# Performance work log

Measured on AMD Instinct MI355X. Metric: run time of the kernel, lower is better.

Reference implementation:

```python
import jax, jax.numpy as jnp
import numpy as np

LAM_U = 0.1
LAM_V = 0.1
LAM_P = 0.1
LAM_Q = 0.1

N_USERS, N_ITEMS, K = 8192, 8192, 256


def _trace(x):
    # PMF repos define trace(x) = sum of squared entries (Frobenius norm^2)
    return jnp.sum(x * x)


def setup_inputs() -> dict:
    key = jax.random.key(0)
    ks = jax.random.split(key, 8)
    R = jax.random.normal(ks[0], (N_USERS, N_ITEMS), jnp.float32)
    R = R * (jax.random.uniform(ks[1], (N_USERS, N_ITEMS)) < 0.05).astype(jnp.float32)
    Y = jax.random.normal(ks[2], (N_USERS, N_ITEMS), jnp.float32)
    Y = Y * (jax.random.uniform(ks[3], (N_USERS, N_ITEMS)) < 0.05).astype(jnp.float32)
    u_features = jax.random.normal(ks[4], (N_USERS, K), jnp.float32)
    v_features = jax.random.normal(ks[5], (N_ITEMS, K), jnp.float32)
    P = jax.random.normal(ks[6], (K, N_USERS), jnp.float32)
    Q = jax.random.normal(ks[7], (K, N_USERS), jnp.float32)
    alpha = jnp.float32(0.5)
    return {"R": R, "u_features": u_features, "v_features": v_features,
            "alpha": alpha, "Y": Y, "P": P, "Q": Q}


def reference(R, u_features, v_features, alpha, Y, P, Q):
    non_zero_mask = (R != 0).astype(jnp.float32)              # [U, I]
    # (P^T * u_features) @ v_features^T : low-rank predicted ratings [U, I]
    predicted = jnp.matmul(P.T * u_features, v_features.T)
    prediction_error = jnp.sum((R - predicted) ** 2 * non_zero_mask) / 2

    non_zero_mask_Y = (Y != 0).astype(jnp.float32)
    predicted_y = jnp.matmul(Q.T * u_features, v_features.T)
    prediction_error_y = alpha * jnp.sum((Y - predicted_y) ** 2 * non_zero_mask_Y) / 2  # computed but NOT returned (faithful to source)

    u_reg = LAM_U * _trace(u_features) / 2
    v_reg = LAM_V * _trace(v_features) / 2
    p_reg = LAM_P * _trace(P) / 2
    q_reg = LAM_Q * _trace(Q) / 2  # computed but not returned (faithful)
    return prediction_error + u_reg + v_reg + p_reg
```

## Files before the change

kernel.cpp:

```cpp
#include <hip/hip_runtime.h>
#include <hip/hip_bf16.h>

typedef __attribute__((ext_vector_type(8))) short short8;
typedef __attribute__((ext_vector_type(4))) float f32x4;

#define N_U 8192
#define N_I 8192
#define KD  256

#define ERR_SLOTS 8192
#define REGA_BASE 8192
#define REGV_BASE 8704
#define SLOTS_END 10752

#define GLD16(g, l) __builtin_amdgcn_global_load_lds( \
    (const __attribute__((address_space(1))) unsigned int*)(unsigned long long)(uintptr_t)(g), \
    (__attribute__((address_space(3))) unsigned int*)(unsigned int)(uintptr_t)(l), 16, 0, 0)

static __device__ __forceinline__ unsigned short f2bf(float x) {
  unsigned u = __builtin_bit_cast(unsigned, x);
  u += 0x7fffu + ((u >> 16) & 1u);
  return (unsigned short)(u >> 16);
}

static __device__ __forceinline__ void block_reduce_store(float v, float* slot) {
  #pragma unroll
  for (int off = 32; off > 0; off >>= 1) v += __shfl_down(v, off, 64);
  __shared__ float red[4];
  int lane = threadIdx.x & 63, wv = threadIdx.x >> 6;
  if (lane == 0) red[wv] = v;
  __syncthreads();
  if (threadIdx.x == 0) *slot = red[0] + red[1] + red[2] + red[3];
}

__global__ __launch_bounds__(256) void pack_a_kernel(
    const float* __restrict__ U, const float* __restrict__ P,
    unsigned short* __restrict__ Abf, float* __restrict__ ws)
{
  __shared__ float Pt[64][65];
  const int u0 = blockIdx.x * 64;
  const int k0 = blockIdx.y * 64;
  const int t = threadIdx.x;
  float ss = 0.f;
  {
    const int ul4 = (t & 15) * 4, klb = t >> 4;
    #pragma unroll
    for (int pass = 0; pass < 4; ++pass) {
      int kl = klb + pass * 16;
      float4 pv = *(const float4*)&P[(size_t)(k0 + kl) * N_U + u0 + ul4];
      Pt[kl][ul4 + 0] = pv.x; Pt[kl][ul4 + 1] = pv.y;
      Pt[kl][ul4 + 2] = pv.z; Pt[kl][ul4 + 3] = pv.w;
      ss += pv.x * pv.x + pv.y * pv.y + pv.z * pv.z + pv.w * pv.w;
    }
  }
  __syncthreads();
  {
    const int k4 = (t & 15) * 4, ulb = t >> 4;
    #pragma unroll
    for (int pass = 0; pass < 4; ++pass) {
      int ul = ulb + pass * 16;
      float4 uv = *(const float4*)&U[(size_t)(u0 + ul) * KD + k0 + k4];
      ss += uv.x * uv.x + uv.y * uv.y + uv.z * uv.z + uv.w * uv.w;
      ushort4 w;
      w.x = f2bf(uv.x * Pt[k4 + 0][ul]);
      w.y = f2bf(uv.y * Pt[k4 + 1][ul]);
      w.z = f2bf(uv.z * Pt[k4 + 2][ul]);
      w.w = f2bf(uv.w * Pt[k4 + 3][ul]);
      *(ushort4*)&Abf[(size_t)(u0 + ul) * KD + k0 + k4] = w;
    }
  }
  block_reduce_store(ss, ws + REGA_BASE + blockIdx.y * 128 + blockIdx.x);
}

__global__ __launch_bounds__(256) void pack_v_kernel(
    const float* __restrict__ V, unsigned short* __restrict__ Vbf,
    float* __restrict__ ws)
{
  size_t i = ((size_t)blockIdx.x * 256 + threadIdx.x) * 4;
  float4 v = *(const float4*)&V[i];
  float ss = v.x * v.x + v.y * v.y + v.z * v.z + v.w * v.w;
  ushort4 w;
  w.x = f2bf(v.x); w.y = f2bf(v.y); w.z = f2bf(v.z); w.w = f2bf(v.w);
  *(ushort4*)&Vbf[i] = w;
  block_reduce_store(ss, ws + REGV_BASE + blockIdx.x);
}

__global__ __launch_bounds__(256) void gemm_loss_kernel(
    const float* __restrict__ R, const unsigned short* __restrict__ Abf,
    const unsigned short* __restrict__ Vbf, float* __restrict__ ws)
{
  __shared__ unsigned short As[2][128 * 32];
  __shared__ unsigned short Bs[2][64 * 32];
  const int tid = threadIdx.x;
  const int wv = tid >> 6, lane = tid & 63;
  const int brow = blockIdx.x, bcol = blockIdx.y;
  const int wr = wv >> 1, wc = wv & 1;

  f32x4 acc[4][2] = {};
  float4 rreg[8];

  const unsigned short* Ag = Abf + (size_t)brow * 128 * KD;
  const unsigned short* Bg = Vbf + (size_t)bcol * 64 * KD;
  const int fa0 = tid, fa1 = tid + 256, fb = tid;
  const int r0 = lane & 15, kc = (lane >> 4) * 8;

  const int row0 = brow * 128 + wr * 64 + (lane & 15);
  const size_t col0 = (size_t)bcol * 64 + wc * 32 + (lane >> 4) * 4;
  const float* Rtile = R + (size_t)row0 * N_I + col0;

#define STAGE(buf, kt) do { \
    GLD16(Ag + ((fa0 >> 2) * KD + (kt) + (fa0 & 3) * 8), &As[buf][fa0 * 8]); \
    GLD16(Ag + ((fa1 >> 2) * KD + (kt) + (fa1 & 3) * 8), &As[buf][fa1 * 8]); \
    GLD16(Bg + ((fb  >> 2) * KD + (kt) + (fb  & 3) * 8), &Bs[buf][fb * 8]);  \
  } while (0)

  STAGE(0, 0);
  asm volatile("s_waitcnt vmcnt(0)" ::: "memory");
  __builtin_amdgcn_s_barrier();

  #pragma unroll
  for (int t = 0; t < 8; ++t) {
    const int cur = t & 1;
    if (t < 7) STAGE(cur ^ 1, (t + 1) * 32);
    rreg[t] = *(const float4*)(Rtile + (size_t)((t >> 1) * 16) * N_I + (t & 1) * 16);

    short8 a[4], b[2];
    #pragma unroll
    for (int m = 0; m < 4; ++m)
      a[m] = *(const short8*)&As[cur][(wr * 64 + m * 16 + r0) * 32 + kc];
    #pragma unroll
    for (int n = 0; n < 2; ++n)
      b[n] = *(const short8*)&Bs[cur][(wc * 32 + n * 16 + r0) * 32 + kc];
    #pragma unroll
    for (int m = 0; m < 4; ++m)
      #pragma unroll
      for (int n = 0; n < 2; ++n)
        acc[m][n] = __builtin_amdgcn_mfma_f32_16x16x32_bf16(b[n], a[m], acc[m][n], 0, 0, 0);

    asm volatile("s_waitcnt lgkmcnt(0) vmcnt(1)" ::: "memory");
    __builtin_amdgcn_s_barrier();
  }
#undef STAGE

  asm volatile("s_waitcnt vmcnt(0)" ::: "memory");
  float lsum = 0.f;
  #pragma unroll
  for (int t = 0; t < 8; ++t) {
    const int m = t >> 1, n = t & 1;
    float4 rv = rreg[t];
    if (rv.x != 0.f) { float d = rv.x - acc[m][n][0]; lsum += d * d; }
    if (rv.y != 0.f) { float d = rv.y - acc[m][n][1]; lsum += d * d; }
    if (rv.z != 0.f) { float d = rv.z - acc[m][n][2]; lsum += d * d; }
    if (rv.w != 0.f) { float d = rv.w - acc[m][n][3]; lsum += d * d; }
  }

  #pragma unroll
  for (int off = 32; off > 0; off >>= 1) lsum += __shfl_down(lsum, off, 64);
  float* red = (float*)As;
  __syncthreads();
  if (lane == 0) red[wv] = lsum;
  __syncthreads();
  if (tid == 0) ws[blockIdx.y * 64 + blockIdx.x] = red[0] + red[1] + red[2] + red[3];
}

__global__ __launch_bounds__(256) void finalize_kernel(
    const float* __restrict__ ws, float* __restrict__ out)
{
  __shared__ float sh[256];
  const int tid = threadIdx.x;
  float e = 0.f, r = 0.f;
  for (int i = tid; i < ERR_SLOTS; i += 256) e += ws[i];
  for (int i = REGA_BASE + tid; i < SLOTS_END; i += 256) r += ws[i];
  sh[tid] = 0.5f * e + 0.05f * r;
  __syncthreads();
  #pragma unroll
  for (int s = 128; s > 0; s >>= 1) {
    if (tid < s) sh[tid] += sh[tid + s];
    __syncthreads();
  }
  if (tid == 0) out[0] = sh[0];
}

extern "C" void kernel_launch(void* const* d_in, const int* in_sizes, int n_in,
                              void* d_out, int out_size, void* d_ws, size_t ws_size,
                              hipStream_t stream) {
  const float* R = (const float*)d_in[0];
  const float* U = (const float*)d_in[1];
  const float* V = (const float*)d_in[2];
  const float* P = (const float*)d_in[5];

  unsigned short* Abf = (unsigned short*)d_ws;
  unsigned short* Vbf = Abf + (size_t)N_U * KD;
  float* ws = (float*)((char*)d_ws + 2 * 4194304);
  float* out = (float*)d_out;

  pack_a_kernel<<<dim3(N_U / 64, KD / 64), 256, 0, stream>>>(U, P, Abf, ws);
  pack_v_kernel<<<dim3((N_I * KD) / (256 * 4)), 256, 0, stream>>>(V, Vbf, ws);
  gemm_loss_kernel<<<dim3(64, 128), 256, 0, stream>>>(R, Abf, Vbf, ws);
  finalize_kernel<<<1, 256, 0, stream>>>(ws, out);
}
```

Measured before the change: 128.9 us.

## Single-buffer GEMM LDS, prefetch all R tiles upfront, per-wave partial sums

The GEMM-loss kernel drops LDS double buffering and uses a single staging buffer guarded by __syncthreads, which halves LDS use and may raise occupancy. All eight R float4 loads are issued at the start so their latency overlaps the whole K loop. The block-level reduction is replaced by each wave writing its own partial sum to the workspace, and the slot counts are enlarged to match. The cost is that global-to-LDS loads no longer overlap MFMA work inside a block, so the kernel relies on other resident blocks to hide that latency.

```diff
diff --git a/kernel.cpp b/kernel.cpp
--- a/kernel.cpp
+++ b/kernel.cpp
@@ -8,10 +8,10 @@
 #define N_I 8192
 #define KD  256
 
-#define ERR_SLOTS 8192
-#define REGA_BASE 8192
-#define REGV_BASE 8704
-#define SLOTS_END 10752
+#define ERR_SLOTS 32768
+#define REGA_BASE 32768
+#define REGV_BASE 33280
+#define SLOTS_END 35328
 
 #define GLD16(g, l) __builtin_amdgcn_global_load_lds( \
     (const __attribute__((address_space(1))) unsigned int*)(unsigned long long)(uintptr_t)(g), \
@@ -89,60 +89,59 @@
     const float* __restrict__ R, const unsigned short* __restrict__ Abf,
     const unsigned short* __restrict__ Vbf, float* __restrict__ ws)
 {
-  __shared__ unsigned short As[2][128 * 32];
-  __shared__ unsigned short Bs[2][64 * 32];
+  __shared__ unsigned short As[128 * 32];
+  __shared__ unsigned short Bs[64 * 32];
   const int tid = threadIdx.x;
   const int wv = tid >> 6, lane = tid & 63;
   const int brow = blockIdx.x, bcol = blockIdx.y;
   const int wr = wv >> 1, wc = wv & 1;
 
   f32x4 acc[4][2] = {};
-  float4 rreg[8];
 
   const unsigned short* Ag = Abf + (size_t)brow * 128 * KD;
   const unsigned short* Bg = Vbf + (size_t)bcol * 64 * KD;
   const int fa0 = tid, fa1 = tid + 256, fb = tid;
   const int r0 = lane & 15, kc = (lane >> 4) * 8;
 
-  const int row0 = brow * 128 + wr * 64 + (lane & 15);
+  const int row0 = brow * 128 + wr * 64 + r0;
   const size_t col0 = (size_t)bcol * 64 + wc * 32 + (lane >> 4) * 4;
   const float* Rtile = R + (size_t)row0 * N_I + col0;
 
-#define STAGE(buf, kt) do { \
-    GLD16(Ag + ((fa0 >> 2) * KD + (kt) + (fa0 & 3) * 8), &As[buf][fa0 * 8]); \
-    GLD16(Ag + ((fa1 >> 2) * KD + (kt) + (fa1 & 3) * 8), &As[buf][fa1 * 8]); \
-    GLD16(Bg + ((fb  >> 2) * KD + (kt) + (fb  & 3) * 8), &Bs[buf][fb * 8]);  \
+#define STAGE(kt) do { \
+    GLD16(Ag + ((fa0 >> 2) * KD + (kt) + (fa0 & 3) * 8), &As[fa0 * 8]); \
+    GLD16(Ag + ((fa1 >> 2) * KD + (kt) + (fa1 & 3) * 8), &As[fa1 * 8]); \
+    GLD16(Bg + ((fb  >> 2) * KD + (kt) + (fb  & 3) * 8), &Bs[fb * 8]);  \
   } while (0)
 
-  STAGE(0, 0);
-  asm volatile("s_waitcnt vmcnt(0)" ::: "memory");
-  __builtin_amdgcn_s_barrier();
+  STAGE(0);
+  float4 rreg[8];
+  #pragma unroll
+  for (int t = 0; t < 8; ++t)
+    rreg[t] = *(const float4*)(Rtile + (size_t)((t >> 1) * 16) * N_I + (t & 1) * 16);
+  asm volatile("" ::: "memory");
 
   #pragma unroll
   for (int t = 0; t < 8; ++t) {
-    const int cur = t & 1;
-    if (t < 7) STAGE(cur ^ 1, (t + 1) * 32);
-    rreg[t] = *(const float4*)(Rtile + (size_t)((t >> 1) * 16) * N_I + (t & 1) * 16);
-
+    if (t) {
+      __syncthreads();
+      STAGE(t * 32);
+    }
+    __syncthreads();
     short8 a[4], b[2];
     #pragma unroll
     for (int m = 0; m < 4; ++m)
-      a[m] = *(const short8*)&As[cur][(wr * 64 + m * 16 + r0) * 32 + kc];
+      a[m] = *(const short8*)&As[(wr * 64 + m * 16 + r0) * 32 + kc];
     #pragma unroll
     for (int n = 0; n < 2; ++n)
-      b[n] = *(const short8*)&Bs[cur][(wc * 32 + n * 16 + r0) * 32 + kc];
+      b[n] = *(const short8*)&Bs[(wc * 32 + n * 16 + r0) * 32 + kc];
     #pragma unroll
     for (int m = 0; m < 4; ++m)
       #pragma unroll
       for (int n = 0; n < 2; ++n)
         acc[m][n] = __builtin_amdgcn_mfma_f32_16x16x32_bf16(b[n], a[m], acc[m][n], 0, 0, 0);
-
-    asm volatile("s_waitcnt lgkmcnt(0) vmcnt(1)" ::: "memory");
-    __builtin_amdgcn_s_barrier();
   }
 #undef STAGE
 
-  asm volatile("s_waitcnt vmcnt(0)" ::: "memory");
   float lsum = 0.f;
   #pragma unroll
   for (int t = 0; t < 8; ++t) {
@@ -156,11 +155,8 @@
 
   #pragma unroll
   for (int off = 32; off > 0; off >>= 1) lsum += __shfl_down(lsum, off, 64);
-  float* red = (float*)As;
-  __syncthreads();
-  if (lane == 0) red[wv] = lsum;
-  __syncthreads();
-  if (tid == 0) ws[blockIdx.y * 64 + blockIdx.x] = red[0] + red[1] + red[2] + red[3];
+  if (lane == 0)
+    ws[((blockIdx.y * 64 + blockIdx.x) << 2) | wv] = lsum;
 }
 
 __global__ __launch_bounds__(256) void finalize_kernel(
```

Result: slower. 148.4 us (+15.2%).
